# Kernel tuning notes

Hardware: AMD Instinct MI355X
Metric: run time of the kernel (lower is better)

## Reference

```python
import jax, jax.numpy as jnp
import numpy as np

B, D, H, N, K, C = 1024, 256, 512, 100000, 96, 10


def setup_inputs() -> dict:
    key = jax.random.key(0)
    ks = jax.random.split(key, 16)
    s = 0.02
    return {
        "x": jax.random.normal(ks[0], (B, D), jnp.float32),
        "candidate_x": jax.random.normal(ks[1], (N, D), jnp.float32),
        "candidate_labels": jax.random.randint(ks[2], (N,), 0, C, jnp.int32),
        "W_enc": jax.random.normal(ks[3], (D, H), jnp.float32) * s,
        "b_enc": jnp.zeros((H,), jnp.float32),
        "W_key": jax.random.normal(ks[4], (H, H), jnp.float32) * s,
        "b_key": jnp.zeros((H,), jnp.float32),
        "W_val": jax.random.normal(ks[5], (H, H), jnp.float32) * s,
        "b_val": jnp.zeros((H,), jnp.float32),
        "E_label": jax.random.normal(ks[6], (C, H), jnp.float32) * s,
        "W_t1": jax.random.normal(ks[7], (H, H), jnp.float32) * s,
        "b_t1": jnp.zeros((H,), jnp.float32),
        "W_t2": jax.random.normal(ks[8], (H, H), jnp.float32) * s,
    }


def reference(x, candidate_x, candidate_labels, W_enc, b_enc, W_key, b_key,
              W_val, b_val, E_label, W_t1, b_t1, W_t2):
    # Encode queries and candidates
    x_enc = x @ W_enc + b_enc                       # [B, H]
    cand_enc = candidate_x @ W_enc + b_enc          # [N, H]
    x_key = x_enc @ W_key + b_key                   # [B, H]
    cand_keys = cand_enc @ W_key + b_key            # [N, H]

    # Negative euclidean distance via GEMM expansion (compute-efficient cdist)
    q2 = jnp.sum(x_key * x_key, axis=-1, keepdims=True)        # [B, 1]
    c2 = jnp.sum(cand_keys * cand_keys, axis=-1)               # [N]
    d2 = q2 + c2[None, :] - 2.0 * (x_key @ cand_keys.T)        # [B, N]
    sim = -jnp.sqrt(jnp.maximum(d2, 0.0))                      # [B, N]

    # Top-k retrieval
    top_sims, top_idx = jax.lax.top_k(sim, K)                  # [B, K]

    cand_vals = cand_enc @ W_val + b_val                       # [N, H]
    label_emb = E_label[candidate_labels]                      # [N, H]

    ctx_keys = cand_keys[top_idx]                              # [B, K, H]
    ctx_labels = label_emb[top_idx]                            # [B, K, H]
    _ = cand_vals[top_idx]  # gathered values (unused by the original math)

    # Attention over retrieved context (softmax of top-k similarities)
    attn = jax.nn.softmax(top_sims, axis=1)                    # [B, K]

    # Correction MLP T (dropout is identity in eval mode)
    diff = x_key[:, None, :] - ctx_keys                        # [B, K, H]
    t_out = jax.nn.relu(diff @ W_t1 + b_t1) @ W_t2             # [B, K, H]

    ctx_vec = jnp.sum(attn[..., None] * (ctx_labels + t_out), axis=1)  # [B, H]
    return x_enc + ctx_vec
```

## Files before the change

kernel.cpp:

```cpp
#include <hip/hip_runtime.h>
#include <cfloat>
#include <cmath>

#define B_ 1024
#define D_ 256
#define H_ 512
#define N_ 100000
#define K_ 96
#define C_ 10
#define SAMP 4096
#define CAPC 4096
#define RCAP 15

typedef __attribute__((ext_vector_type(8))) short bf16x8;
typedef __attribute__((ext_vector_type(4))) float f32x4;

__device__ __forceinline__ float bf2f(ushort h) {
    union { unsigned u; float f; } v; v.u = ((unsigned)h) << 16; return v.f;
}
__device__ __forceinline__ ushort f2bf(float f) {
    union { float f; unsigned u; } v; v.f = f;
    unsigned u = v.u;
    unsigned r = (u + 0x7fffu + ((u >> 16) & 1u)) >> 16;
    return (ushort)r;
}
__device__ __forceinline__ unsigned f2key(float f) {
    unsigned u = __float_as_uint(f);
    return (u & 0x80000000u) ? ~u : (u | 0x80000000u);
}
__device__ __forceinline__ float d2_of(float acc, float q2, float c2) {
    return fmaxf(fmaf(-2.f, acc, q2 + c2), 0.f);
}

#define GLDS(g, l)                                                            \
    __builtin_amdgcn_global_load_lds(                                         \
        (const __attribute__((address_space(1))) void*)(g),                   \
        (__attribute__((address_space(3))) void*)(l), 16, 0, 0)

template <int RELU>
__global__ __launch_bounds__(256) void gemm_nn(const float* __restrict__ A,
                                               const float* __restrict__ Bm,
                                               const float* __restrict__ bias,
                                               float* __restrict__ Cm,
                                               int M, int N, int Kd) {
    __shared__ float sA[16][68];
    __shared__ float sB[16][64];
    const int t  = threadIdx.x;
    const int tx = t & 15, ty = t >> 4;
    const int m0 = blockIdx.y * 64;
    const int n0 = blockIdx.x * 64;
    const int lr = t >> 2;
    const int lk = (t & 3) << 2;
    const int bk = t >> 4;
    const int bn = (t & 15) << 2;

    float acc[4][4] = {};
    for (int k0 = 0; k0 < Kd; k0 += 16) {
        float4 av = make_float4(0.f, 0.f, 0.f, 0.f);
        if (m0 + lr < M)
            av = *(const float4*)(A + (size_t)(m0 + lr) * Kd + k0 + lk);
        sA[lk + 0][lr] = av.x; sA[lk + 1][lr] = av.y;
        sA[lk + 2][lr] = av.z; sA[lk + 3][lr] = av.w;
        float4 bv = *(const float4*)(Bm + (size_t)(k0 + bk) * N + n0 + bn);
        *(float4*)&sB[bk][bn] = bv;
        __syncthreads();
#pragma unroll
        for (int kk = 0; kk < 16; ++kk) {
            float4 a4 = *(const float4*)&sA[kk][ty << 2];
            float4 b4 = *(const float4*)&sB[kk][tx << 2];
            float ar[4] = {a4.x, a4.y, a4.z, a4.w};
            float br[4] = {b4.x, b4.y, b4.z, b4.w};
#pragma unroll
            for (int i = 0; i < 4; ++i)
#pragma unroll
                for (int j = 0; j < 4; ++j)
                    acc[i][j] = fmaf(ar[i], br[j], acc[i][j]);
        }
        __syncthreads();
    }
#pragma unroll
    for (int i = 0; i < 4; ++i) {
        int row = m0 + (ty << 2) + i;
        if (row < M) {
            int col = n0 + (tx << 2);
            float b0 = 0.f, b1 = 0.f, b2 = 0.f, b3 = 0.f;
            if (bias) { b0 = bias[col]; b1 = bias[col + 1]; b2 = bias[col + 2]; b3 = bias[col + 3]; }
            float4 o;
            o.x = acc[i][0] + b0; o.y = acc[i][1] + b1;
            o.z = acc[i][2] + b2; o.w = acc[i][3] + b3;
            if (RELU) {
                o.x = fmaxf(o.x, 0.f); o.y = fmaxf(o.y, 0.f);
                o.z = fmaxf(o.z, 0.f); o.w = fmaxf(o.w, 0.f);
            }
            *(float4*)(Cm + (size_t)row * N + col) = o;
        }
    }
}

template <int MODE, int SWZ>
__global__ __launch_bounds__(256) void gemm_nt(const ushort* __restrict__ A,
                                               const ushort* __restrict__ Bv,
                                               const float* __restrict__ bias,
                                               const float* __restrict__ q2v,
                                               const float* __restrict__ c2v,
                                               const float* __restrict__ thrv,
                                               float* __restrict__ candV,
                                               int* __restrict__ candI,
                                               int* __restrict__ cnt,
                                               void* __restrict__ Cout,
                                               int M, int Nlim, int K,
                                               int ldc, int nvalid, int per) {
    int m0, n0;
    if (SWZ == 0) {
        m0 = blockIdx.y * 128; n0 = blockIdx.x * 128;
    } else if (SWZ == 1) {
        int bid = blockIdx.x;
        int xcd = bid & 7, slot = bid >> 3;
        m0 = (slot & 7) * 128;
        n0 = (xcd * per + (slot >> 3)) * 128;
        if (n0 >= nvalid || m0 >= M) return;
    } else {
        int bid = blockIdx.x;
        int xcd = bid & 7, slot = bid >> 3;
        n0 = (slot & 3) * 128;
        m0 = (xcd * per + (slot >> 2)) * 128;
        if (m0 >= M) return;
    }

    __shared__ __align__(16) char smem[16896];
    ushort* sA = (ushort*)smem;
    ushort* sB = (ushort*)(smem + 8192);
    const int t = threadIdx.x;
    const int lane = t & 63, w = t >> 6;
    const int wm = w & 1, wn = w >> 1;

    f32x4 acc[4][4];
#pragma unroll
    for (int i = 0; i < 4; ++i)
#pragma unroll
        for (int j = 0; j < 4; ++j)
            acc[i][j] = (f32x4){0.f, 0.f, 0.f, 0.f};

    const int la = lane & 15, lk = lane >> 4;
    const int aoff = (wm * 64 + la) * 64 + lk * 16;
    const int boff = (wn * 64 + la) * 64 + lk * 16;
    const int r_ = t >> 2, cc_ = (t & 3);

    for (int k0 = 0; k0 < K; k0 += 32) {
#pragma unroll
        for (int q = 0; q < 2; ++q) {
            int r = r_ + q * 64;
            int ar = m0 + r; ar = (ar < M) ? ar : (M - 1);
            GLDS(A + (size_t)ar * K + k0 + cc_ * 8, (char*)sA + (q * 256 + t) * 16);
            int br = n0 + r; br = (br < Nlim) ? br : (Nlim - 1);
            GLDS(Bv + (size_t)br * K + k0 + cc_ * 8, (char*)sB + (q * 256 + t) * 16);
        }
        __syncthreads();
        bf16x8 af[4], bfr[4];
#pragma unroll
        for (int i = 0; i < 4; ++i)
            af[i] = *(const bf16x8*)((const char*)sA + aoff + i * 1024);
#pragma unroll
        for (int j = 0; j < 4; ++j)
            bfr[j] = *(const bf16x8*)((const char*)sB + boff + j * 1024);
#pragma unroll
        for (int i = 0; i < 4; ++i)
#pragma unroll
            for (int j = 0; j < 4; ++j)
                acc[i][j] = __builtin_amdgcn_mfma_f32_16x16x32_bf16(
                    af[i], bfr[j], acc[i][j], 0, 0, 0);
        __syncthreads();
    }

    const int rl = (lane >> 4) * 4, cl = lane & 15;

    if (MODE == 5) {
        float* stV = (float*)smem;
        int*   stI = (int*)(smem + 7680);
        int*   stC = (int*)(smem + 16384);
        for (int r = t; r < 128; r += 256) stC[r] = 0;
        __syncthreads();
#pragma unroll
        for (int i = 0; i < 4; ++i) {
#pragma unroll
            for (int v = 0; v < 4; ++v) {
                int rloc = wm * 64 + i * 16 + rl + v;
                int gr = m0 + rloc;
                float q2b = q2v[gr];
                float th = thrv[gr];
#pragma unroll
                for (int j = 0; j < 4; ++j) {
                    int gc = n0 + wn * 64 + j * 16 + cl;
                    if (gc < nvalid) {
                        float d2 = d2_of(acc[i][j][v], q2b, c2v[gc]);
                        if (d2 <= th) {
                            int p = atomicAdd(&stC[rloc], 1);
                            if (p < RCAP) {
                                stV[rloc * RCAP + p] = d2;
                                stI[rloc * RCAP + p] = gc;
                            } else {
                                int gp = atomicAdd(&cnt[gr], 1);
                                if (gp < CAPC) {
                                    candV[(size_t)gr * CAPC + gp] = d2;
                                    candI[(size_t)gr * CAPC + gp] = gc;
                                }
                            }
                        }
                    }
                }
            }
        }
        __syncthreads();
        for (int r = t; r < 128; r += 256) {
            int n = stC[r]; if (n > RCAP) n = RCAP;
            if (n > 0) {
                int gr = m0 + r;
                int gb = atomicAdd(&cnt[gr], n);
                for (int q = 0; q < n; ++q) {
                    int pos = gb + q;
                    if (pos < CAPC) {
                        candV[(size_t)gr * CAPC + pos] = stV[r * RCAP + q];
                        candI[(size_t)gr * CAPC + pos] = stI[r * RCAP + q];
                    }
                }
            }
        }
        return;
    }

#pragma unroll
    for (int i = 0; i < 4; ++i) {
#pragma unroll
        for (int j = 0; j < 4; ++j) {
            int gc = n0 + wn * 64 + j * 16 + cl;
#pragma unroll
            for (int v = 0; v < 4; ++v) {
                int gr = m0 + wm * 64 + i * 16 + rl + v;
                if (gr < M && gc < nvalid) {
                    float val = acc[i][j][v];
                    if (MODE == 2) {
                        ((float*)Cout)[(size_t)gr * ldc + gc] = val;
                    } else {
                        if (MODE == 1 || MODE == 3) val += bias[gc];
                        if (MODE == 1) val = fmaxf(val, 0.f);
                        ((ushort*)Cout)[(size_t)gr * ldc + gc] = f2bf(val);
                    }
                }
            }
        }
    }
}

__global__ __launch_bounds__(256) void thr_select(const float* __restrict__ S,
                                                  int ld,
                                                  const float* __restrict__ q2v,
                                                  const float* __restrict__ c2v,
                                                  float* __restrict__ thrArr) {
    __shared__ unsigned keys[SAMP];
    __shared__ int hist[256];
    __shared__ int sel[2];
    const int b = blockIdx.x, t = threadIdx.x;
    const float q2b = q2v[b];
    for (int i = t; i < SAMP; i += 256)
        keys[i] = ~f2key(d2_of(S[(size_t)b * ld + i], q2b, c2v[i]));
    __syncthreads();
    unsigned prefix = 0, mask = 0;
    int rank = K_;
    for (int shift = 24; shift >= 0; shift -= 8) {
        hist[t & 255] = 0;
        __syncthreads();
        for (int i = t; i < SAMP; i += 256) {
            unsigned k = keys[i];
            if ((k & mask) == prefix) atomicAdd(&hist[(k >> shift) & 255], 1);
        }
        __syncthreads();
        if (t == 0) {
            int r = rank, d = 255;
            for (; d > 0; --d) { int c = hist[d]; if (r - c <= 0) break; r -= c; }
            sel[0] = d; sel[1] = (r < 1) ? 1 : r;
        }
        __syncthreads();
        prefix |= ((unsigned)sel[0]) << shift;
        rank = sel[1];
        mask |= (0xFFu << shift);
        __syncthreads();
    }
    if (t == 0) {
        unsigned key = ~prefix;
        thrArr[b] = __uint_as_float(key & 0x7FFFFFFFu);
    }
}

__global__ __launch_bounds__(256) void final_select(const float* __restrict__ candV,
                                                    const int* __restrict__ candI,
                                                    const int* __restrict__ cnt,
                                                    float* __restrict__ topV,
                                                    int* __restrict__ topI) {
    __shared__ unsigned keys[CAPC];
    __shared__ int hist[256];
    __shared__ int sel[2];
    __shared__ int poscnt, eqcnt;
    const int b = blockIdx.x, t = threadIdx.x;
    int n = cnt[b]; if (n > CAPC) n = CAPC;
    for (int i = t; i < n; i += 256)
        keys[i] = ~f2key(candV[(size_t)b * CAPC + i]);
    __syncthreads();
    unsigned prefix = 0, mask = 0;
    int rank = K_;
    for (int shift = 24; shift >= 0; shift -= 8) {
        hist[t & 255] = 0;
        __syncthreads();
        for (int i = t; i < n; i += 256) {
            unsigned k = keys[i];
            if ((k & mask) == prefix) atomicAdd(&hist[(k >> shift) & 255], 1);
        }
        __syncthreads();
        if (t == 0) {
            int r = rank, d = 255;
            for (; d > 0; --d) { int c = hist[d]; if (r - c <= 0) break; r -= c; }
            sel[0] = d; sel[1] = (r < 1) ? 1 : r;
        }
        __syncthreads();
        prefix |= ((unsigned)sel[0]) << shift;
        rank = sel[1];
        mask |= (0xFFu << shift);
        __syncthreads();
    }
    unsigned kth = prefix;
    if (t == 0) { poscnt = 0; eqcnt = 0; }
    __syncthreads();
    for (int i = t; i < n; i += 256) {
        if (keys[i] > kth) {
            int p = atomicAdd(&poscnt, 1);
            topV[b * K_ + p] = candV[(size_t)b * CAPC + i];
            topI[b * K_ + p] = candI[(size_t)b * CAPC + i];
        }
    }
    __syncthreads();
    int base = poscnt;
    for (int i = t; i < n; i += 256) {
        if (keys[i] == kth) {
            int p = atomicAdd(&eqcnt, 1);
            if (base + p < K_) {
                topV[b * K_ + base + p] = candV[(size_t)b * CAPC + i];
                topI[b * K_ + base + p] = candI[(size_t)b * CAPC + i];
            }
        }
    }
}

__global__ void init_cnt(int* cnt) {
    int i = blockIdx.x * 256 + threadIdx.x;
    if (i < B_) cnt[i] = 0;
}

__global__ void conv_f2b(const float* __restrict__ in, ushort* __restrict__ out, int n) {
    int i = (blockIdx.x * 256 + threadIdx.x) * 4;
    int stride = gridDim.x * 256 * 4;
    for (; i < n; i += stride) {
        float4 v = *(const float4*)(in + i);
        ushort4 o;
        o.x = f2bf(v.x); o.y = f2bf(v.y); o.z = f2bf(v.z); o.w = f2bf(v.w);
        *(ushort4*)(out + i) = o;
    }
}

__global__ __launch_bounds__(256) void transpose_f2b(const float* __restrict__ in,
                                                     ushort* __restrict__ out,
                                                     int R, int Cn) {
    __shared__ float tile[32][33];
    int bx = blockIdx.x * 32, by = blockIdx.y * 32;
    int tx = threadIdx.x & 31, ty = threadIdx.x >> 5;
    int x = bx + tx;
#pragma unroll
    for (int dy = 0; dy < 32; dy += 8) {
        int y = by + ty + dy;
        if (x < Cn && y < R) tile[ty + dy][tx] = in[(size_t)y * Cn + x];
    }
    __syncthreads();
    int ox = by + tx;
#pragma unroll
    for (int dy = 0; dy < 32; dy += 8) {
        int oy = bx + ty + dy;
        if (ox < R && oy < Cn) out[(size_t)oy * R + ox] = f2bf(tile[tx][ty + dy]);
    }
}

__global__ __launch_bounds__(64) void rowsq_b(const ushort* __restrict__ X,
                                              float* __restrict__ outv) {
    const int r = blockIdx.x, t = threadIdx.x;
    const ushort* p = X + (size_t)r * H_;
    ushort4 a = *(const ushort4*)(p + t * 4);
    ushort4 b = *(const ushort4*)(p + 256 + t * 4);
    float ax = bf2f(a.x), ay = bf2f(a.y), az = bf2f(a.z), aw = bf2f(a.w);
    float bx = bf2f(b.x), by = bf2f(b.y), bz = bf2f(b.z), bw = bf2f(b.w);
    float v = ax * ax + ay * ay + az * az + aw * aw +
              bx * bx + by * by + bz * bz + bw * bw;
    for (int off = 32; off > 0; off >>= 1) v += __shfl_down(v, off);
    if (t == 0) outv[r] = v;
}

__global__ __launch_bounds__(64) void q2x_k(const ushort* __restrict__ Xb,
                                            const float* __restrict__ Xf,
                                            const float* __restrict__ bc,
                                            float* __restrict__ outv) {
    const int r = blockIdx.x, t = threadIdx.x;
    const ushort* p  = Xb + (size_t)r * H_ + t * 8;
    const float*  xf = Xf + (size_t)r * H_ + t * 8;
    float nrm = 0.f, dot = 0.f;
#pragma unroll
    for (int j = 0; j < 8; ++j) {
        float v = bf2f(p[j]);
        nrm = fmaf(v, v, nrm);
        dot = fmaf(xf[j], bc[t * 8 + j], dot);
    }
    for (int off = 32; off > 0; off >>= 1) {
        nrm += __shfl_down(nrm, off);
        dot += __shfl_down(dot, off);
    }
    if (t == 0) outv[r] = nrm - 2.f * dot;
}

__global__ void bcomb_k(const float* __restrict__ b_enc,
                        const float* __restrict__ W_key,
                        const float* __restrict__ b_key,
                        float* __restrict__ b_comb) {
    int h = blockIdx.x * 256 + threadIdx.x;
    if (h >= H_) return;
    float acc = b_key[h];
    for (int m = 0; m < H_; ++m)
        acc = fmaf(b_enc[m], W_key[(size_t)m * H_ + h], acc);
    b_comb[h] = acc;
}

__global__ __launch_bounds__(128) void softmax_k(const float* __restrict__ topVal,
                                                 float* __restrict__ attn) {
    __shared__ float red[128];
    const int b = blockIdx.x, t = threadIdx.x;
    float v = (t < K_) ? -sqrtf(topVal[b * K_ + t]) : -FLT_MAX;
    red[t] = v; __syncthreads();
    for (int s = 64; s > 0; s >>= 1) {
        if (t < s) red[t] = fmaxf(red[t], red[t + s]);
        __syncthreads();
    }
    float m = red[0]; __syncthreads();
    float e = (t < K_) ? expf(v - m) : 0.f;
    red[t] = e; __syncthreads();
    for (int s = 64; s > 0; s >>= 1) {
        if (t < s) red[t] += red[t + s];
        __syncthreads();
    }
    float ssum = red[0];
    if (t < K_) attn[b * K_ + t] = e / ssum;
}

__global__ __launch_bounds__(128) void gather_diff_b(const float* __restrict__ XK,
                                                     const ushort* __restrict__ CK,
                                                     const int* __restrict__ topI,
                                                     ushort* __restrict__ diff,
                                                     int b0) {
    const int r = blockIdx.x;
    const int b = b0 + r / K_;
    const int idx = topI[b * K_ + (r % K_)];
    const int t = threadIdx.x;
    float4 xv = *(const float4*)(XK + (size_t)b * H_ + t * 4);
    ushort4 cv = *(const ushort4*)(CK + (size_t)idx * H_ + t * 4);
    ushort4 o;
    o.x = f2bf(xv.x - bf2f(cv.x));
    o.y = f2bf(xv.y - bf2f(cv.y));
    o.z = f2bf(xv.z - bf2f(cv.z));
    o.w = f2bf(xv.w - bf2f(cv.w));
    *(ushort4*)(diff + (size_t)r * H_ + t * 4) = o;
}

__global__ __launch_bounds__(256) void wsum_h(const float* __restrict__ attn,
                                              const ushort* __restrict__ h,
                                              ushort* __restrict__ hw, int b0) {
    const int bl = blockIdx.x;
    const int b = b0 + bl;
    const int t = threadIdx.x;
    float a0 = 0.f, a1 = 0.f;
    const float* ap = attn + b * K_;
    for (int k = 0; k < K_; ++k) {
        float w = ap[k];
        const ushort* hr = h + (size_t)(bl * K_ + k) * H_;
        a0 = fmaf(w, bf2f(hr[t]), a0);
        a1 = fmaf(w, bf2f(hr[t + 256]), a1);
    }
    hw[(size_t)b * H_ + t]       = f2bf(a0);
    hw[(size_t)b * H_ + t + 256] = f2bf(a1);
}

__global__ __launch_bounds__(256) void final_out(const float* __restrict__ attn,
                                                 const int* __restrict__ topI,
                                                 const int* __restrict__ labels,
                                                 const float* __restrict__ E,
                                                 const float* __restrict__ tsum,
                                                 const float* __restrict__ xe,
                                                 float* __restrict__ out) {
    const int b = blockIdx.x, t = threadIdx.x;
    float a0 = 0.f, a1 = 0.f;
    for (int k = 0; k < K_; ++k) {
        float w = attn[b * K_ + k];
        int idx = topI[b * K_ + k];
        int lab = labels[idx];
        const float* el = E + (size_t)lab * H_;
        a0 = fmaf(w, el[t], a0);
        a1 = fmaf(w, el[t + 256], a1);
    }
    out[(size_t)b * H_ + t] =
        xe[(size_t)b * H_ + t] + a0 + tsum[(size_t)b * H_ + t];
    out[(size_t)b * H_ + t + 256] =
        xe[(size_t)b * H_ + t + 256] + a1 + tsum[(size_t)b * H_ + t + 256];
}

extern "C" void kernel_launch(void* const* d_in, const int* in_sizes, int n_in,
                              void* d_out, int out_size, void* d_ws, size_t ws_size,
                              hipStream_t stream) {
    const float* x      = (const float*)d_in[0];
    const float* cx     = (const float*)d_in[1];
    const int*   labels = (const int*)d_in[2];
    const float* W_enc  = (const float*)d_in[3];
    const float* b_enc  = (const float*)d_in[4];
    const float* W_key  = (const float*)d_in[5];
    const float* b_key  = (const float*)d_in[6];
    const float* E_label = (const float*)d_in[9];
    const float* W_t1   = (const float*)d_in[10];
    const float* b_t1   = (const float*)d_in[11];
    const float* W_t2   = (const float*)d_in[12];
    float* out = (float*)d_out;

    char* base = (char*)d_ws;
    size_t off = 0;
    auto take = [&](size_t n) -> char* {
        char* p = base + off;
        off = (off + n + 255) & ~(size_t)255;
        return p;
    };
    float*  Wc    = (float*)take((size_t)D_ * H_ * 4);
    float*  bc    = (float*)take((size_t)H_ * 4);
    ushort* WcT   = (ushort*)take((size_t)H_ * D_ * 2);
    ushort* Wcb   = (ushort*)take((size_t)D_ * H_ * 2);
    ushort* Wt1T  = (ushort*)take((size_t)H_ * H_ * 2);
    ushort* Wt2T  = (ushort*)take((size_t)H_ * H_ * 2);
    float*  xe    = (float*)take((size_t)B_ * H_ * 4);
    float*  xk    = (float*)take((size_t)B_ * H_ * 4);
    ushort* xkb   = (ushort*)take((size_t)B_ * H_ * 2);
    ushort* xprojb= (ushort*)take((size_t)B_ * D_ * 2);
    float*  q2x   = (float*)take((size_t)B_ * 4);
    ushort* ckb   = (ushort*)take((size_t)N_ * H_ * 2);
    float*  c2    = (float*)take((size_t)N_ * 4);
    float*  topV  = (float*)take((size_t)B_ * K_ * 4);
    int*    topI  = (int*)take((size_t)B_ * K_ * 4);
    float*  thr   = (float*)take((size_t)B_ * 4);
    float*  attn  = (float*)take((size_t)B_ * K_ * 4);
    int*    cnt   = (int*)take((size_t)B_ * 4);
    float*  candV = (float*)take((size_t)B_ * CAPC * 4);
    int*    candI = (int*)take((size_t)B_ * CAPC * 4);
    ushort* hwAll = (ushort*)take((size_t)B_ * H_ * 2);
    float*  tsum  = (float*)take((size_t)B_ * H_ * 4);
    char*   big   = base + off;
    size_t rem = (ws_size > off) ? (ws_size - off) : 0;

    ushort* cxb = (ushort*)big;
    float* simSmall = (float*)candV;

    long long bcq = (long long)(rem / ((size_t)K_ * H_ * 2 * 2));
    if (bcq > B_) bcq = B_;
    if (bcq < 1) bcq = 1;
    int Bc = (int)bcq;

    {
        dim3 g(H_ / 64, D_ / 64);
        gemm_nn<0><<<g, 256, 0, stream>>>(W_enc, W_key, nullptr, Wc, D_, H_, H_);
        bcomb_k<<<(H_ + 255) / 256, 256, 0, stream>>>(b_enc, W_key, b_key, bc);
        dim3 gt1((H_ + 31) / 32, (D_ + 31) / 32);
        transpose_f2b<<<gt1, 256, 0, stream>>>(Wc, WcT, D_, H_);
        conv_f2b<<<128, 256, 0, stream>>>(Wc, Wcb, D_ * H_);
        dim3 gt2((H_ + 31) / 32, (H_ + 31) / 32);
        transpose_f2b<<<gt2, 256, 0, stream>>>(W_t1, Wt1T, H_, H_);
        transpose_f2b<<<gt2, 256, 0, stream>>>(W_t2, Wt2T, H_, H_);
    }
    {
        dim3 gx(H_ / 64, B_ / 64);
        gemm_nn<0><<<gx, 256, 0, stream>>>(x, W_enc, b_enc, xe, B_, H_, D_);
        gemm_nn<0><<<gx, 256, 0, stream>>>(x, Wc, bc, xk, B_, H_, D_);
        conv_f2b<<<1024, 256, 0, stream>>>(xk, xkb, B_ * H_);
        conv_f2b<<<2048, 256, 0, stream>>>(cx, cxb, N_ * D_);
        dim3 gp(D_ / 128, B_ / 128);
        gemm_nt<0, 0><<<gp, 256, 0, stream>>>(
            xkb, Wcb, nullptr, nullptr, nullptr, nullptr, nullptr, nullptr,
            nullptr, xprojb, B_, D_, H_, D_, D_, 0);
        q2x_k<<<B_, 64, 0, stream>>>(xkb, xk, bc, q2x);
    }
    {
        int mt = (N_ + 127) / 128;
        int mper = (mt + 7) / 8;
        gemm_nt<3, 2><<<8 * mper * 4, 256, 0, stream>>>(
            cxb, WcT, bc, nullptr, nullptr, nullptr, nullptr, nullptr, nullptr,
            ckb, N_, H_, D_, H_, H_, mper);
    }
    rowsq_b<<<N_, 64, 0, stream>>>(ckb, c2);

    {
        int nper = (SAMP / 128 + 7) / 8;
        gemm_nt<2, 1><<<64 * nper, 256, 0, stream>>>(
            xprojb, cxb, nullptr, nullptr, nullptr, nullptr, nullptr, nullptr,
            nullptr, simSmall, B_, N_, D_, SAMP, SAMP, nper);
        thr_select<<<B_, 256, 0, stream>>>(simSmall, SAMP, q2x, c2, thr);
    }
    init_cnt<<<(B_ + 255) / 256, 256, 0, stream>>>(cnt);
    {
        int NT = (N_ + 127) / 128;
        int nper = (NT + 7) / 8;
        gemm_nt<5, 1><<<64 * nper, 256, 0, stream>>>(
            xprojb, cxb, nullptr, q2x, c2, thr, candV, candI, cnt,
            nullptr, B_, N_, D_, 0, N_, nper);
    }
    final_select<<<B_, 256, 0, stream>>>(candV, candI, cnt, topV, topI);
    softmax_k<<<B_, 128, 0, stream>>>(topV, attn);

    ushort* diffB = (ushort*)big;
    ushort* hB = (ushort*)(big + (size_t)Bc * K_ * H_ * 2);
    for (int b0 = 0; b0 < B_; b0 += Bc) {
        int bcn = min(Bc, B_ - b0);
        int Mrows = bcn * K_;
        gather_diff_b<<<Mrows, 128, 0, stream>>>(xk, ckb, topI, diffB, b0);
        int mt4 = (Mrows + 127) / 128;
        int mper4 = (mt4 + 7) / 8;
        gemm_nt<1, 2><<<8 * mper4 * 4, 256, 0, stream>>>(
            diffB, Wt1T, b_t1, nullptr, nullptr, nullptr, nullptr, nullptr,
            nullptr, hB, Mrows, H_, H_, H_, H_, mper4);
        wsum_h<<<bcn, 256, 0, stream>>>(attn, hB, hwAll, b0);
    }
    {
        dim3 g(H_ / 128, B_ / 128);
        gemm_nt<2, 0><<<g, 256, 0, stream>>>(
            hwAll, Wt2T, nullptr, nullptr, nullptr, nullptr, nullptr, nullptr,
            nullptr, tsum, B_, H_, H_, H_, H_, 0);
    }
    final_out<<<B_, 256, 0, stream>>>(attn, topI, labels, E_label, tsum, xe, out);
}
```

Baseline: 929.3 us.

## Replace tiled sim-filter GEMM with persistent strip kernel overlapping MFMA and filtering

```diff
diff --git a/kernel.cpp b/kernel.cpp
--- a/kernel.cpp
+++ b/kernel.cpp
@@ -11,6 +11,8 @@
 #define SAMP 4096
 #define CAPC 4096
 #define RCAP 15
+#define NCT 1563
+#define NSTRIP 32
 
 typedef __attribute__((ext_vector_type(8))) short bf16x8;
 typedef __attribute__((ext_vector_type(4))) float f32x4;
@@ -36,6 +38,8 @@
     __builtin_amdgcn_global_load_lds(                                         \
         (const __attribute__((address_space(1))) void*)(g),                   \
         (__attribute__((address_space(3))) void*)(l), 16, 0, 0)
+
+#define FENCE() asm volatile("" ::: "memory")
 
 template <int RELU>
 __global__ __launch_bounds__(256) void gemm_nn(const float* __restrict__ A,
@@ -101,12 +105,6 @@
 __global__ __launch_bounds__(256) void gemm_nt(const ushort* __restrict__ A,
                                                const ushort* __restrict__ Bv,
                                                const float* __restrict__ bias,
-                                               const float* __restrict__ q2v,
-                                               const float* __restrict__ c2v,
-                                               const float* __restrict__ thrv,
-                                               float* __restrict__ candV,
-                                               int* __restrict__ candI,
-                                               int* __restrict__ cnt,
                                                void* __restrict__ Cout,
                                                int M, int Nlim, int K,
                                                int ldc, int nvalid, int per) {
@@ -174,60 +172,6 @@
 
     const int rl = (lane >> 4) * 4, cl = lane & 15;
 
-    if (MODE == 5) {
-        float* stV = (float*)smem;
-        int*   stI = (int*)(smem + 7680);
-        int*   stC = (int*)(smem + 16384);
-        for (int r = t; r < 128; r += 256) stC[r] = 0;
-        __syncthreads();
-#pragma unroll
-        for (int i = 0; i < 4; ++i) {
-#pragma unroll
-            for (int v = 0; v < 4; ++v) {
-                int rloc = wm * 64 + i * 16 + rl + v;
-                int gr = m0 + rloc;
-                float q2b = q2v[gr];
-                float th = thrv[gr];
-#pragma unroll
-                for (int j = 0; j < 4; ++j) {
-                    int gc = n0 + wn * 64 + j * 16 + cl;
-                    if (gc < nvalid) {
-                        float d2 = d2_of(acc[i][j][v], q2b, c2v[gc]);
-                        if (d2 <= th) {
-                            int p = atomicAdd(&stC[rloc], 1);
-                            if (p < RCAP) {
-                                stV[rloc * RCAP + p] = d2;
-                                stI[rloc * RCAP + p] = gc;
-                            } else {
-                                int gp = atomicAdd(&cnt[gr], 1);
-                                if (gp < CAPC) {
-                                    candV[(size_t)gr * CAPC + gp] = d2;
-                                    candI[(size_t)gr * CAPC + gp] = gc;
-                                }
-                            }
-                        }
-                    }
-                }
-            }
-        }
-        __syncthreads();
-        for (int r = t; r < 128; r += 256) {
-            int n = stC[r]; if (n > RCAP) n = RCAP;
-            if (n > 0) {
-                int gr = m0 + r;
-                int gb = atomicAdd(&cnt[gr], n);
-                for (int q = 0; q < n; ++q) {
-                    int pos = gb + q;
-                    if (pos < CAPC) {
-                        candV[(size_t)gr * CAPC + pos] = stV[r * RCAP + q];
-                        candI[(size_t)gr * CAPC + pos] = stI[r * RCAP + q];
-                    }
-                }
-            }
-        }
-        return;
-    }
-
 #pragma unroll
     for (int i = 0; i < 4; ++i) {
 #pragma unroll
@@ -248,6 +192,166 @@
                 }
             }
         }
+    }
+}
+
+#define MFMA_(a, b, c) __builtin_amdgcn_mfma_f32_16x16x32_bf16(a, b, c, 0, 0, 0)
+
+#define FILT_PIECE(ACCP, PN, KF)                                              \
+    {                                                                         \
+        int gc_ = (PN) + ((KF) & 3) * 16 + la;                                \
+        float c2c_ = (gc_ < nvalid) ? c2v[gc_] : 3.0e38f;                     \
+        _Pragma("unroll")                                                     \
+        for (int v_ = 0; v_ < 4; ++v_) {                                      \
+            float d2_ = d2_of(ACCP[(KF) >> 2][(KF) & 3][v_],                  \
+                              q2r[((KF) >> 2) * 4 + v_], c2c_);               \
+            if (d2_ <= thrr[((KF) >> 2) * 4 + v_]) {                          \
+                int gm_ = gmr[((KF) >> 2) * 4 + v_];                          \
+                int pp_ = atomicAdd(&cnt[gm_], 1);                            \
+                if (pp_ < CAPC) {                                             \
+                    candV[(size_t)gm_ * CAPC + pp_] = d2_;                    \
+                    candI[(size_t)gm_ * CAPC + pp_] = gc_;                    \
+                }                                                             \
+            }                                                                 \
+        }                                                                     \
+        ACCP[(KF) >> 2][(KF) & 3] = (f32x4){0.f, 0.f, 0.f, 0.f};              \
+    }
+
+#define CHUNK_BODY(ACCC, ACCP, BUFOFF, PN, HASPREV)                           \
+    do {                                                                      \
+        const char* bp_ = sB + (BUFOFF) + la * 512;                           \
+        _Pragma("unroll")                                                     \
+        for (int kf = 0; kf < 8; ++kf) {                                      \
+            int g_ = (((kf * 4 + lk) ^ sw) << 4);                             \
+            bf16x8 b0_ = *(const bf16x8*)(bp_ + g_);                          \
+            bf16x8 b1_ = *(const bf16x8*)(bp_ + 8192 + g_);                   \
+            bf16x8 b2_ = *(const bf16x8*)(bp_ + 16384 + g_);                  \
+            bf16x8 b3_ = *(const bf16x8*)(bp_ + 24576 + g_);                  \
+            ACCC[0][0] = MFMA_(aR[0][kf], b0_, ACCC[0][0]);                   \
+            ACCC[0][1] = MFMA_(aR[0][kf], b1_, ACCC[0][1]);                   \
+            ACCC[0][2] = MFMA_(aR[0][kf], b2_, ACCC[0][2]);                   \
+            ACCC[0][3] = MFMA_(aR[0][kf], b3_, ACCC[0][3]);                   \
+            ACCC[1][0] = MFMA_(aR[1][kf], b0_, ACCC[1][0]);                   \
+            ACCC[1][1] = MFMA_(aR[1][kf], b1_, ACCC[1][1]);                   \
+            ACCC[1][2] = MFMA_(aR[1][kf], b2_, ACCC[1][2]);                   \
+            ACCC[1][3] = MFMA_(aR[1][kf], b3_, ACCC[1][3]);                   \
+            if (HASPREV) FILT_PIECE(ACCP, PN, kf)                             \
+        }                                                                     \
+    } while (0)
+
+#define POST_STAGE(CC)                                                        \
+    do {                                                                      \
+        FENCE(); __builtin_amdgcn_s_barrier();                                \
+        int cs_ = (CC) + 2;                                                   \
+        if (cs_ < c1) {                                                       \
+            stage_b(cs_, (((CC)-c0) & 1) * 32768);                            \
+            asm volatile("s_waitcnt vmcnt(8)" ::: "memory");                  \
+        } else {                                                              \
+            asm volatile("s_waitcnt vmcnt(0)" ::: "memory");                  \
+        }                                                                     \
+        __builtin_amdgcn_s_barrier(); FENCE();                                \
+    } while (0)
+
+__global__ __launch_bounds__(256, 1) void sim_filter(
+    const ushort* __restrict__ A, const ushort* __restrict__ Bv,
+    const float* __restrict__ q2v, const float* __restrict__ c2v,
+    const float* __restrict__ thrv, float* __restrict__ candV,
+    int* __restrict__ candI, int* __restrict__ cnt, int nvalid) {
+    __shared__ __align__(16) char smem[131072];
+    char* sA = smem;
+    char* sB = smem + 65536;
+
+    const int t = threadIdx.x;
+    const int lane = t & 63, w = t >> 6;
+    const int la = lane & 15, lk = lane >> 4, sw = la & 7;
+
+    const int bid = blockIdx.x;
+    const int mt = bid >> 5;
+    const int strip = ((bid & 7) << 2) | ((bid >> 3) & 3);
+    const int m0 = mt << 7;
+    const int c0 = strip * NCT / NSTRIP;
+    const int c1 = (strip + 1) * NCT / NSTRIP;
+
+    const int trow = t >> 5;
+    const int sw8 = ((t & 31) ^ (trow & 7)) << 3;
+
+    auto stage_b = [&](int ck, int bufoff) {
+        char* d = sB + bufoff + t * 16;
+        size_t nb = (size_t)ck << 6;
+#pragma unroll
+        for (int i = 0; i < 8; ++i) {
+            long rg = (long)nb + i * 8 + trow;
+            if (rg >= nvalid) rg = nvalid - 1;
+            GLDS(Bv + (size_t)rg * 256 + sw8, d + i * 4096);
+        }
+    };
+
+    {
+        char* dA = sA + t * 16;
+#pragma unroll
+        for (int i = 0; i < 16; ++i) {
+            int row = m0 + i * 8 + trow;
+            GLDS(A + (size_t)row * 256 + sw8, dA + i * 4096);
+        }
+    }
+    stage_b(c0, 0);
+    int cpre = (c0 + 1 < c1) ? c0 + 1 : c0;
+    stage_b(cpre, 32768);
+    asm volatile("s_waitcnt vmcnt(8)" ::: "memory");
+    __builtin_amdgcn_s_barrier(); FENCE();
+
+    bf16x8 aR[2][8];
+    {
+        const char* ap = sA + (w * 32 + la) * 512;
+#pragma unroll
+        for (int mf = 0; mf < 2; ++mf)
+#pragma unroll
+            for (int ks = 0; ks < 8; ++ks)
+                aR[mf][ks] = *(const bf16x8*)(ap + mf * 8192 +
+                                              (((ks * 4 + lk) ^ sw) << 4));
+    }
+
+    int gmr[8]; float q2r[8], thrr[8];
+#pragma unroll
+    for (int mf = 0; mf < 2; ++mf)
+#pragma unroll
+        for (int v = 0; v < 4; ++v) {
+            int gm = m0 + w * 32 + mf * 16 + lk * 4 + v;
+            gmr[mf * 4 + v] = gm;
+            q2r[mf * 4 + v] = q2v[gm];
+            thrr[mf * 4 + v] = thrv[gm];
+        }
+
+    f32x4 acc0[2][4], acc1[2][4];
+#pragma unroll
+    for (int i = 0; i < 2; ++i)
+#pragma unroll
+        for (int j = 0; j < 4; ++j) {
+            acc0[i][j] = (f32x4){0.f, 0.f, 0.f, 0.f};
+            acc1[i][j] = (f32x4){0.f, 0.f, 0.f, 0.f};
+        }
+
+    CHUNK_BODY(acc0, acc1, 0, 0, false);
+    POST_STAGE(c0);
+    int pn = c0 * 64;
+    int c = c0 + 1;
+    for (; c + 1 < c1; c += 2) {
+        CHUNK_BODY(acc1, acc0, 32768, pn, true);
+        POST_STAGE(c);
+        pn = c * 64;
+        CHUNK_BODY(acc0, acc1, 0, pn, true);
+        POST_STAGE(c + 1);
+        pn = (c + 1) * 64;
+    }
+    if (c < c1) {
+        CHUNK_BODY(acc1, acc0, 32768, pn, true);
+        POST_STAGE(c);
+        pn = c * 64;
+#pragma unroll
+        for (int p8 = 0; p8 < 8; ++p8) FILT_PIECE(acc1, pn, p8);
+    } else {
+#pragma unroll
+        for (int p8 = 0; p8 < 8; ++p8) FILT_PIECE(acc0, pn, p8);
     }
 }
 
@@ -589,34 +693,26 @@
         conv_f2b<<<2048, 256, 0, stream>>>(cx, cxb, N_ * D_);
         dim3 gp(D_ / 128, B_ / 128);
         gemm_nt<0, 0><<<gp, 256, 0, stream>>>(
-            xkb, Wcb, nullptr, nullptr, nullptr, nullptr, nullptr, nullptr,
-            nullptr, xprojb, B_, D_, H_, D_, D_, 0);
+            xkb, Wcb, nullptr, xprojb, B_, D_, H_, D_, D_, 0);
         q2x_k<<<B_, 64, 0, stream>>>(xkb, xk, bc, q2x);
     }
     {
         int mt = (N_ + 127) / 128;
         int mper = (mt + 7) / 8;
         gemm_nt<3, 2><<<8 * mper * 4, 256, 0, stream>>>(
-            cxb, WcT, bc, nullptr, nullptr, nullptr, nullptr, nullptr, nullptr,
-            ckb, N_, H_, D_, H_, H_, mper);
+            cxb, WcT, bc, ckb, N_, H_, D_, H_, H_, mper);
     }
     rowsq_b<<<N_, 64, 0, stream>>>(ckb, c2);
 
     {
         int nper = (SAMP / 128 + 7) / 8;
         gemm_nt<2, 1><<<64 * nper, 256, 0, stream>>>(
-            xprojb, cxb, nullptr, nullptr, nullptr, nullptr, nullptr, nullptr,
-            nullptr, simSmall, B_, N_, D_, SAMP, SAMP, nper);
+            xprojb, cxb, nullptr, simSmall, B_, N_, D_, SAMP, SAMP, nper);
         thr_select<<<B_, 256, 0, stream>>>(simSmall, SAMP, q2x, c2, thr);
     }
     init_cnt<<<(B_ + 255) / 256, 256, 0, stream>>>(cnt);
-    {
-        int NT = (N_ + 127) / 128;
-        int nper = (NT + 7) / 8;
-        gemm_nt<5, 1><<<64 * nper, 256, 0, stream>>>(
-            xprojb, cxb, nullptr, q2x, c2, thr, candV, candI, cnt,
-            nullptr, B_, N_, D_, 0, N_, nper);
-    }
+    sim_filter<<<8 * NSTRIP, 256, 0, stream>>>(
+        xprojb, cxb, q2x, c2, thr, candV, candI, cnt, N_);
     final_select<<<B_, 256, 0, stream>>>(candV, candI, cnt, topV, topI);
     softmax_k<<<B_, 128, 0, stream>>>(topV, attn);
 
@@ -629,15 +725,13 @@
         int mt4 = (Mrows + 127) / 128;
         int mper4 = (mt4 + 7) / 8;
         gemm_nt<1, 2><<<8 * mper4 * 4, 256, 0, stream>>>(
-            diffB, Wt1T, b_t1, nullptr, nullptr, nullptr, nullptr, nullptr,
-            nullptr, hB, Mrows, H_, H_, H_, H_, mper4);
+            diffB, Wt1T, b_t1, hB, Mrows, H_, H_, H_, H_, mper4);
         wsum_h<<<bcn, 256, 0, stream>>>(attn, hB, hwAll, b0);
     }
     {
         dim3 g(H_ / 128, B_ / 128);
         gemm_nt<2, 0><<<g, 256, 0, stream>>>(
-            hwAll, Wt2T, nullptr, nullptr, nullptr, nullptr, nullptr, nullptr,
-            nullptr, tsum, B_, H_, H_, H_, H_, 0);
+            hwAll, Wt2T, nullptr, tsum, B_, H_, H_, H_, H_, 0);
     }
     final_out<<<B_, 256, 0, stream>>>(attn, topI, labels, E_label, tsum, xe, out);
 }
```

Result: slower. 1.483 ms (+59.6%).

## Replace fused distance-filter GEMM with dedicated kernel looping over four N-tiles per block

Applied to the files above, without the earlier changes.

```diff
diff --git a/kernel.cpp b/kernel.cpp
--- a/kernel.cpp
+++ b/kernel.cpp
@@ -10,7 +10,10 @@
 #define C_ 10
 #define SAMP 4096
 #define CAPC 4096
-#define RCAP 15
+#define NT3 782
+#define NSUB 4
+#define NGRP ((NT3 + NSUB - 1) / NSUB)
+#define RCAP3 32
 
 typedef __attribute__((ext_vector_type(8))) short bf16x8;
 typedef __attribute__((ext_vector_type(4))) float f32x4;
@@ -101,12 +104,6 @@
 __global__ __launch_bounds__(256) void gemm_nt(const ushort* __restrict__ A,
                                                const ushort* __restrict__ Bv,
                                                const float* __restrict__ bias,
-                                               const float* __restrict__ q2v,
-                                               const float* __restrict__ c2v,
-                                               const float* __restrict__ thrv,
-                                               float* __restrict__ candV,
-                                               int* __restrict__ candI,
-                                               int* __restrict__ cnt,
                                                void* __restrict__ Cout,
                                                int M, int Nlim, int K,
                                                int ldc, int nvalid, int per) {
@@ -174,60 +171,6 @@
 
     const int rl = (lane >> 4) * 4, cl = lane & 15;
 
-    if (MODE == 5) {
-        float* stV = (float*)smem;
-        int*   stI = (int*)(smem + 7680);
-        int*   stC = (int*)(smem + 16384);
-        for (int r = t; r < 128; r += 256) stC[r] = 0;
-        __syncthreads();
-#pragma unroll
-        for (int i = 0; i < 4; ++i) {
-#pragma unroll
-            for (int v = 0; v < 4; ++v) {
-                int rloc = wm * 64 + i * 16 + rl + v;
-                int gr = m0 + rloc;
-                float q2b = q2v[gr];
-                float th = thrv[gr];
-#pragma unroll
-                for (int j = 0; j < 4; ++j) {
-                    int gc = n0 + wn * 64 + j * 16 + cl;
-                    if (gc < nvalid) {
-                        float d2 = d2_of(acc[i][j][v], q2b, c2v[gc]);
-                        if (d2 <= th) {
-                            int p = atomicAdd(&stC[rloc], 1);
-                            if (p < RCAP) {
-                                stV[rloc * RCAP + p] = d2;
-                                stI[rloc * RCAP + p] = gc;
-                            } else {
-                                int gp = atomicAdd(&cnt[gr], 1);
-                                if (gp < CAPC) {
-                                    candV[(size_t)gr * CAPC + gp] = d2;
-                                    candI[(size_t)gr * CAPC + gp] = gc;
-                                }
-                            }
-                        }
-                    }
-                }
-            }
-        }
-        __syncthreads();
-        for (int r = t; r < 128; r += 256) {
-            int n = stC[r]; if (n > RCAP) n = RCAP;
-            if (n > 0) {
-                int gr = m0 + r;
-                int gb = atomicAdd(&cnt[gr], n);
-                for (int q = 0; q < n; ++q) {
-                    int pos = gb + q;
-                    if (pos < CAPC) {
-                        candV[(size_t)gr * CAPC + pos] = stV[r * RCAP + q];
-                        candI[(size_t)gr * CAPC + pos] = stI[r * RCAP + q];
-                    }
-                }
-            }
-        }
-        return;
-    }
-
 #pragma unroll
     for (int i = 0; i < 4; ++i) {
 #pragma unroll
@@ -245,6 +188,134 @@
                         if (MODE == 1) val = fmaxf(val, 0.f);
                         ((ushort*)Cout)[(size_t)gr * ldc + gc] = f2bf(val);
                     }
+                }
+            }
+        }
+    }
+}
+
+__global__ __launch_bounds__(256) void filt128(const ushort* __restrict__ A,
+                                               const ushort* __restrict__ Bv,
+                                               const float* __restrict__ q2v,
+                                               const float* __restrict__ c2v,
+                                               const float* __restrict__ thrv,
+                                               float* __restrict__ candV,
+                                               int* __restrict__ candI,
+                                               int* __restrict__ cnt,
+                                               int M, int K, int nvalid) {
+    __shared__ __align__(16) char smem[16896];
+    __shared__ float stV[128][RCAP3];
+    __shared__ int   stI[128][RCAP3];
+    __shared__ int   stC[128];
+    ushort* sA = (ushort*)smem;
+    ushort* sB = (ushort*)(smem + 8192);
+    const int t = threadIdx.x;
+    const int lane = t & 63, w = t >> 6;
+    const int wm = w & 1, wn = w >> 1;
+    const int la = lane & 15, lk = lane >> 4;
+    const int aoff = (wm * 64 + la) * 64 + lk * 16;
+    const int boff = (wn * 64 + la) * 64 + lk * 16;
+    const int r_ = t >> 2, cc_ = (t & 3);
+    const int rl = lk * 4, cl = la;
+
+    const int wu = (blockIdx.x & 7) * NGRP + (blockIdx.x >> 3);
+    const int mt = wu & 7, grp = wu >> 3;
+    const int m0 = mt * 128;
+
+    for (int r = t; r < 128; r += 256) stC[r] = 0;
+
+    float q2r[4][4], thrr[4][4];
+#pragma unroll
+    for (int i = 0; i < 4; ++i)
+#pragma unroll
+        for (int v = 0; v < 4; ++v) {
+            int gr = m0 + wm * 64 + i * 16 + rl + v;
+            q2r[i][v] = q2v[gr];
+            thrr[i][v] = thrv[gr];
+        }
+
+    for (int s = 0; s < NSUB; ++s) {
+        int ntile = grp * NSUB + s;
+        if (ntile >= NT3) break;
+        int n0 = ntile * 128;
+
+        f32x4 acc[4][4];
+#pragma unroll
+        for (int i = 0; i < 4; ++i)
+#pragma unroll
+            for (int j = 0; j < 4; ++j)
+                acc[i][j] = (f32x4){0.f, 0.f, 0.f, 0.f};
+
+        for (int k0 = 0; k0 < K; k0 += 32) {
+#pragma unroll
+            for (int q = 0; q < 2; ++q) {
+                int r = r_ + q * 64;
+                int ar = m0 + r; ar = (ar < M) ? ar : (M - 1);
+                GLDS(A + (size_t)ar * K + k0 + cc_ * 8,
+                     (char*)sA + (q * 256 + t) * 16);
+                int br = n0 + r; br = (br < nvalid) ? br : (nvalid - 1);
+                GLDS(Bv + (size_t)br * K + k0 + cc_ * 8,
+                     (char*)sB + (q * 256 + t) * 16);
+            }
+            __syncthreads();
+            bf16x8 af[4], bfr[4];
+#pragma unroll
+            for (int i = 0; i < 4; ++i)
+                af[i] = *(const bf16x8*)((const char*)sA + aoff + i * 1024);
+#pragma unroll
+            for (int j = 0; j < 4; ++j)
+                bfr[j] = *(const bf16x8*)((const char*)sB + boff + j * 1024);
+#pragma unroll
+            for (int i = 0; i < 4; ++i)
+#pragma unroll
+                for (int j = 0; j < 4; ++j)
+                    acc[i][j] = __builtin_amdgcn_mfma_f32_16x16x32_bf16(
+                        af[i], bfr[j], acc[i][j], 0, 0, 0);
+            __syncthreads();
+        }
+
+#pragma unroll
+        for (int i = 0; i < 4; ++i) {
+#pragma unroll
+            for (int j = 0; j < 4; ++j) {
+                int gc = n0 + wn * 64 + j * 16 + cl;
+                if (gc < nvalid) {
+                    float c2c = c2v[gc];
+#pragma unroll
+                    for (int v = 0; v < 4; ++v) {
+                        float d2 = d2_of(acc[i][j][v], q2r[i][v], c2c);
+                        if (d2 <= thrr[i][v]) {
+                            int rloc = wm * 64 + i * 16 + rl + v;
+                            int p = atomicAdd(&stC[rloc], 1);
+                            if (p < RCAP3) {
+                                stV[rloc][p] = d2;
+                                stI[rloc][p] = gc;
+                            } else {
+                                int gr = m0 + rloc;
+                                int gp = atomicAdd(&cnt[gr], 1);
+                                if (gp < CAPC) {
+                                    candV[(size_t)gr * CAPC + gp] = d2;
+                                    candI[(size_t)gr * CAPC + gp] = gc;
+                                }
+                            }
+                        }
+                    }
+                }
+            }
+        }
+    }
+
+    __syncthreads();
+    for (int r = t; r < 128; r += 256) {
+        int n = stC[r]; if (n > RCAP3) n = RCAP3;
+        if (n > 0) {
+            int gr = m0 + r;
+            int gb = atomicAdd(&cnt[gr], n);
+            for (int q = 0; q < n; ++q) {
+                int pos = gb + q;
+                if (pos < CAPC) {
+                    candV[(size_t)gr * CAPC + pos] = stV[r][q];
+                    candI[(size_t)gr * CAPC + pos] = stI[r][q];
                 }
             }
         }
@@ -589,34 +660,26 @@
         conv_f2b<<<2048, 256, 0, stream>>>(cx, cxb, N_ * D_);
         dim3 gp(D_ / 128, B_ / 128);
         gemm_nt<0, 0><<<gp, 256, 0, stream>>>(
-            xkb, Wcb, nullptr, nullptr, nullptr, nullptr, nullptr, nullptr,
-            nullptr, xprojb, B_, D_, H_, D_, D_, 0);
+            xkb, Wcb, nullptr, xprojb, B_, D_, H_, D_, D_, 0);
         q2x_k<<<B_, 64, 0, stream>>>(xkb, xk, bc, q2x);
     }
     {
         int mt = (N_ + 127) / 128;
         int mper = (mt + 7) / 8;
         gemm_nt<3, 2><<<8 * mper * 4, 256, 0, stream>>>(
-            cxb, WcT, bc, nullptr, nullptr, nullptr, nullptr, nullptr, nullptr,
-            ckb, N_, H_, D_, H_, H_, mper);
+            cxb, WcT, bc, ckb, N_, H_, D_, H_, H_, mper);
     }
     rowsq_b<<<N_, 64, 0, stream>>>(ckb, c2);
 
     {
         int nper = (SAMP / 128 + 7) / 8;
         gemm_nt<2, 1><<<64 * nper, 256, 0, stream>>>(
-            xprojb, cxb, nullptr, nullptr, nullptr, nullptr, nullptr, nullptr,
-            nullptr, simSmall, B_, N_, D_, SAMP, SAMP, nper);
+            xprojb, cxb, nullptr, simSmall, B_, N_, D_, SAMP, SAMP, nper);
         thr_select<<<B_, 256, 0, stream>>>(simSmall, SAMP, q2x, c2, thr);
     }
     init_cnt<<<(B_ + 255) / 256, 256, 0, stream>>>(cnt);
-    {
-        int NT = (N_ + 127) / 128;
-        int nper = (NT + 7) / 8;
-        gemm_nt<5, 1><<<64 * nper, 256, 0, stream>>>(
-            xprojb, cxb, nullptr, q2x, c2, thr, candV, candI, cnt,
-            nullptr, B_, N_, D_, 0, N_, nper);
-    }
+    filt128<<<8 * NGRP, 256, 0, stream>>>(
+        xprojb, cxb, q2x, c2, thr, candV, candI, cnt, B_, D_, N_);
     final_select<<<B_, 256, 0, stream>>>(candV, candI, cnt, topV, topI);
     softmax_k<<<B_, 128, 0, stream>>>(topV, attn);
 
@@ -629,15 +692,13 @@
         int mt4 = (Mrows + 127) / 128;
         int mper4 = (mt4 + 7) / 8;
         gemm_nt<1, 2><<<8 * mper4 * 4, 256, 0, stream>>>(
-            diffB, Wt1T, b_t1, nullptr, nullptr, nullptr, nullptr, nullptr,
-            nullptr, hB, Mrows, H_, H_, H_, H_, mper4);
+            diffB, Wt1T, b_t1, hB, Mrows, H_, H_, H_, H_, mper4);
         wsum_h<<<bcn, 256, 0, stream>>>(attn, hB, hwAll, b0);
     }
     {
         dim3 g(H_ / 128, B_ / 128);
         gemm_nt<2, 0><<<g, 256, 0, stream>>>(
-            hwAll, Wt2T, nullptr, nullptr, nullptr, nullptr, nullptr, nullptr,
-            nullptr, tsum, B_, H_, H_, H_, H_, 0);
+            hwAll, Wt2T, nullptr, tsum, B_, H_, H_, H_, H_, 0);
     }
     final_out<<<B_, 256, 0, stream>>>(attn, topI, labels, E_label, tsum, xe, out);
 }
```

Result: slower. 994.2 us (+7.0%).

## Double-buffer LDS tiles in bf16 MFMA GEMM to overlap loads with compute

Applied to the files above, without the earlier changes.

```diff
diff --git a/kernel.cpp b/kernel.cpp
--- a/kernel.cpp
+++ b/kernel.cpp
@@ -36,6 +36,8 @@
     __builtin_amdgcn_global_load_lds(                                         \
         (const __attribute__((address_space(1))) void*)(g),                   \
         (__attribute__((address_space(3))) void*)(l), 16, 0, 0)
+
+#define FENCE() asm volatile("" ::: "memory")
 
 template <int RELU>
 __global__ __launch_bounds__(256) void gemm_nn(const float* __restrict__ A,
@@ -127,9 +129,7 @@
         if (m0 >= M) return;
     }
 
-    __shared__ __align__(16) char smem[16896];
-    ushort* sA = (ushort*)smem;
-    ushort* sB = (ushort*)(smem + 8192);
+    __shared__ __align__(16) char smem[32768];
     const int t = threadIdx.x;
     const int lane = t & 63, w = t >> 6;
     const int wm = w & 1, wn = w >> 1;
@@ -146,30 +146,52 @@
     const int boff = (wn * 64 + la) * 64 + lk * 16;
     const int r_ = t >> 2, cc_ = (t & 3);
 
-    for (int k0 = 0; k0 < K; k0 += 32) {
+    auto stage = [&](int k0, int buf) {
 #pragma unroll
         for (int q = 0; q < 2; ++q) {
             int r = r_ + q * 64;
             int ar = m0 + r; ar = (ar < M) ? ar : (M - 1);
-            GLDS(A + (size_t)ar * K + k0 + cc_ * 8, (char*)sA + (q * 256 + t) * 16);
+            GLDS(A + (size_t)ar * K + k0 + cc_ * 8,
+                 (char*)smem + buf * 8192 + (q * 256 + t) * 16);
             int br = n0 + r; br = (br < Nlim) ? br : (Nlim - 1);
-            GLDS(Bv + (size_t)br * K + k0 + cc_ * 8, (char*)sB + (q * 256 + t) * 16);
-        }
-        __syncthreads();
+            GLDS(Bv + (size_t)br * K + k0 + cc_ * 8,
+                 (char*)smem + 16384 + buf * 8192 + (q * 256 + t) * 16);
+        }
+    };
+
+    stage(0, 0);
+    int cur = 0;
+    for (int k0 = 0; k0 < K; k0 += 32) {
+        if (k0 + 32 < K) {
+            stage(k0 + 32, cur ^ 1);
+            FENCE();
+            asm volatile("s_waitcnt vmcnt(4)" ::: "memory");
+        } else {
+            FENCE();
+            asm volatile("s_waitcnt vmcnt(0)" ::: "memory");
+        }
+        __builtin_amdgcn_s_barrier(); FENCE();
+
         bf16x8 af[4], bfr[4];
+        const char* pA = (const char*)smem + cur * 8192 + aoff;
+        const char* pB = (const char*)smem + 16384 + cur * 8192 + boff;
 #pragma unroll
         for (int i = 0; i < 4; ++i)
-            af[i] = *(const bf16x8*)((const char*)sA + aoff + i * 1024);
+            af[i] = *(const bf16x8*)(pA + i * 1024);
 #pragma unroll
         for (int j = 0; j < 4; ++j)
-            bfr[j] = *(const bf16x8*)((const char*)sB + boff + j * 1024);
+            bfr[j] = *(const bf16x8*)(pB + j * 1024);
 #pragma unroll
         for (int i = 0; i < 4; ++i)
 #pragma unroll
             for (int j = 0; j < 4; ++j)
                 acc[i][j] = __builtin_amdgcn_mfma_f32_16x16x32_bf16(
                     af[i], bfr[j], acc[i][j], 0, 0, 0);
-        __syncthreads();
+
+        FENCE();
+        asm volatile("s_waitcnt lgkmcnt(0)" ::: "memory");
+        __builtin_amdgcn_s_barrier(); FENCE();
+        cur ^= 1;
     }
 
     const int rl = (lane >> 4) * 4, cl = lane & 15;
@@ -177,7 +199,7 @@
     if (MODE == 5) {
         float* stV = (float*)smem;
         int*   stI = (int*)(smem + 7680);
-        int*   stC = (int*)(smem + 16384);
+        int*   stC = (int*)(smem + 15360);
         for (int r = t; r < 128; r += 256) stC[r] = 0;
         __syncthreads();
 #pragma unroll
```

Result: faster. 893.9 us (-3.8%).
